# Kernel optimization log

Hardware: AMD Instinct MI355X
Metric: run time of the kernel (lower is better)

Reference implementation:

```python
import jax, jax.numpy as jnp
import numpy as np

D = 1024
H = 16
HD = D // H


def setup_inputs() -> dict:
    key = jax.random.key(0)
    ks = jax.random.split(key, 11)
    B, S = 4, 1024
    s = 0.02
    return {
        "q": jax.random.normal(ks[0], (B, S, D), jnp.float32),
        "k": jax.random.normal(ks[1], (B, S, D), jnp.float32),
        "v": jax.random.normal(ks[2], (B, S, D), jnp.float32),
        "Wq": jax.random.normal(ks[3], (D, D), jnp.float32) * s,
        "bq": jnp.zeros((D,), jnp.float32),
        "Wk": jax.random.normal(ks[4], (D, D), jnp.float32) * s,
        "bk": jnp.zeros((D,), jnp.float32),
        "Wv": jax.random.normal(ks[5], (D, D), jnp.float32) * s,
        "bv": jnp.zeros((D,), jnp.float32),
        "Wo": jax.random.normal(ks[6], (D, D), jnp.float32) * s,
        "bo": jnp.zeros((D,), jnp.float32),
    }


def _split_heads(x):
    # [B, S, D] -> [B, H, S, HD]
    B, S, _ = x.shape
    return x.reshape(B, S, H, HD).transpose(0, 2, 1, 3)


def reference(q, k, v, Wq, bq, Wk, bk, Wv, bv, Wo, bo):
    # Projections followed by ReLU (faithful to the original module)
    qh = _split_heads(jax.nn.relu(q @ Wq + bq))
    kh = _split_heads(jax.nn.relu(k @ Wk + bk))
    vh = _split_heads(jax.nn.relu(v @ Wv + bv))
    # NOTE: original scales by sqrt(input_dim), not sqrt(head_dim)
    scale = 1.0 / jnp.sqrt(jnp.float32(D))
    scores = jnp.einsum("bhsd,bhtd->bhst", qh, kh) * scale  # [B,H,S,S]
    weights = jax.nn.softmax(scores, axis=-1)  # dropout is identity in eval
    attn = jnp.einsum("bhst,bhtd->bhsd", weights, vh)  # [B,H,S,HD]
    B, _, S, _ = attn.shape
    attn = attn.transpose(0, 2, 1, 3).reshape(B, S, D)
    return attn @ Wo + bo
```

## Files before the change

kernel.cpp:

```cpp
#include <hip/hip_runtime.h>
#include <math.h>

#define Dm 1024
#define Hn 16
#define HDn 64
#define Sn 1024

typedef __attribute__((ext_vector_type(8))) __bf16 bf16x8;
typedef __attribute__((ext_vector_type(4))) float floatx4;

__device__ __forceinline__ void async_ld16(void* lds, const void* g) {
    __builtin_amdgcn_global_load_lds(
        (const __attribute__((address_space(1))) void*)g,
        (__attribute__((address_space(3))) void*)lds,
        16, 0, 0);
}

struct PrepArgs {
    const float* qkv[3];
    __bf16*      qkv_o[3];
    const float* W[4];
    __bf16*      WT[4];
    float*       out_zero;
};

__global__ __launch_bounds__(256) void prep_kernel(PrepArgs a)
{
    __shared__ float sT[64][65];
    const int z = blockIdx.z, x = blockIdx.x, tid = threadIdx.x;

    if (z < 3) {
        const float* src = a.qkv[z];
        __bf16* dst = a.qkv_o[z];
        const int lin = x * 256 + tid;
        const float4 v0 = ((const float4*)src)[lin * 2];
        const float4 v1 = ((const float4*)src)[lin * 2 + 1];
        bf16x8 o;
        o[0] = (__bf16)v0.x; o[1] = (__bf16)v0.y; o[2] = (__bf16)v0.z; o[3] = (__bf16)v0.w;
        o[4] = (__bf16)v1.x; o[5] = (__bf16)v1.y; o[6] = (__bf16)v1.z; o[7] = (__bf16)v1.w;
        ((bf16x8*)dst)[lin] = o;
    } else if (z < 7) {
        if (x >= 256) return;
        const float* W = a.W[z - 3];
        __bf16* O = a.WT[z - 3];
        const int bi = (x >> 4) * 64, bj = (x & 15) * 64;
        const int colr = tid & 63, rowg = tid >> 6;
        #pragma unroll
        for (int i = 0; i < 16; ++i) {
            const int kk = i * 4 + rowg;
            sT[kk][colr] = W[(size_t)(bi + kk) * Dm + bj + colr];
        }
        __syncthreads();
        #pragma unroll
        for (int i = 0; i < 16; ++i) {
            const int rn = i * 4 + rowg;
            O[(size_t)(bj + rn) * Dm + bi + colr] = (__bf16)sT[colr][rn];
        }
    } else {
        float4* o = (float4*)a.out_zero;
        const int i = (x * 256 + tid) * 2;
        const float4 zz = make_float4(0.f, 0.f, 0.f, 0.f);
        o[i] = zz;
        o[i + 1] = zz;
    }
}

struct GemmArgs {
    const __bf16* X[3];
    const __bf16* WT[3];
    const float*  bias[3];
    void*         out[3];
    int   layout[3];
    float esc[3];
};

__global__ __launch_bounds__(256) void gemm_bf16_kernel(GemmArgs args)
{
    __shared__ __align__(16) __bf16 sA[128 * 64];
    __shared__ __align__(16) __bf16 sB[128 * 64];

    const int z = blockIdx.z;
    const __bf16* __restrict__ Xb  = args.X[z];
    const __bf16* __restrict__ WTb = args.WT[z];
    const float*  __restrict__ bias = args.bias[z];
    void* __restrict__ outp = args.out[z];
    const int layout = args.layout[z];
    const float escale = args.esc[z];

    const int tid = threadIdx.x;
    const int id = blockIdx.x + (blockIdx.y << 3);
    const int bm = (((id & 7) << 2) | (id >> 6)) * 128;
    const int bn = ((id >> 3) & 7) * 128;

    const int lane = tid & 63;
    const int wave = tid >> 6;
    const int wm = (wave & 1) * 64;
    const int wn = (wave >> 1) * 64;
    const int l15 = lane & 15, quad = lane >> 4;

    floatx4 acc[4][4];
    #pragma unroll
    for (int mi = 0; mi < 4; ++mi)
        #pragma unroll
        for (int ni = 0; ni < 4; ++ni)
            acc[mi][ni] = (floatx4){0.f, 0.f, 0.f, 0.f};

    const __bf16* gA[4];
    const __bf16* gB[4];
    #pragma unroll
    for (int j = 0; j < 4; ++j) {
        const int c = j * 256 + tid;
        const int row = c >> 3;
        const int q = (c & 7) ^ (row & 7);
        gA[j] = Xb  + (size_t)(bm + row) * Dm + q * 8;
        gB[j] = WTb + (size_t)(bn + row) * Dm + q * 8;
    }
    char* const lA = (char*)sA + (tid & 192) * 16;
    char* const lB = (char*)sB + (tid & 192) * 16;

    for (int kt = 0; kt < Dm; kt += 64) {
        #pragma unroll
        for (int j = 0; j < 4; ++j) {
            async_ld16(lA + j * 4096, gA[j] + kt);
            async_ld16(lB + j * 4096, gB[j] + kt);
        }
        __syncthreads();

        #pragma unroll
        for (int ks = 0; ks < 2; ++ks) {
            bf16x8 af[4], bfr[4];
            #pragma unroll
            for (int mi = 0; mi < 4; ++mi) {
                const int r = wm + mi * 16 + l15;
                af[mi] = *(const bf16x8*)(sA + r * 64 + ((((ks << 2) + quad) ^ (r & 7)) * 8));
            }
            #pragma unroll
            for (int ni = 0; ni < 4; ++ni) {
                const int r = wn + ni * 16 + l15;
                bfr[ni] = *(const bf16x8*)(sB + r * 64 + ((((ks << 2) + quad) ^ (r & 7)) * 8));
            }
            #pragma unroll
            for (int mi = 0; mi < 4; ++mi)
                #pragma unroll
                for (int ni = 0; ni < 4; ++ni)
                    acc[mi][ni] = __builtin_amdgcn_mfma_f32_16x16x32_bf16(
                        af[mi], bfr[ni], acc[mi][ni], 0, 0, 0);
        }
        __syncthreads();
    }

    #pragma unroll
    for (int mi = 0; mi < 4; ++mi) {
        #pragma unroll
        for (int ni = 0; ni < 4; ++ni) {
            const int n = bn + wn + ni * 16 + l15;
            const float bv = bias[n];
            const int h = n >> 6, d = n & 63;
            #pragma unroll
            for (int reg = 0; reg < 4; ++reg) {
                const int m = bm + wm + mi * 16 + quad * 4 + reg;
                const int b = m >> 10, s = m & 1023;
                float v = fmaxf(acc[mi][ni][reg] + bv, 0.0f) * escale;
                if (layout == 0)
                    ((__bf16*)outp)[((size_t)(b * Hn + h) * 1024 + s) * 64 + d] = (__bf16)v;
                else
                    ((__bf16*)outp)[((size_t)(b * Hn + h) * 64 + d) * 1024 + s] = (__bf16)v;
            }
        }
    }
}

__global__ __launch_bounds__(256) void gemm_splitk_kernel(
    const __bf16* __restrict__ Xb, const __bf16* __restrict__ WTb,
    const float* __restrict__ bias, float* __restrict__ outp)
{
    __shared__ __align__(16) __bf16 sA[128 * 64];
    __shared__ __align__(16) __bf16 sB[128 * 64];

    const int tid = threadIdx.x;
    const int kz = blockIdx.z;
    const int id = blockIdx.x + (blockIdx.y << 3);
    const int bm = (((id & 7) << 2) | (id >> 6)) * 128;
    const int bn = ((id >> 3) & 7) * 128;

    const int lane = tid & 63;
    const int wave = tid >> 6;
    const int wm = (wave & 1) * 64;
    const int wn = (wave >> 1) * 64;
    const int l15 = lane & 15, quad = lane >> 4;

    floatx4 acc[4][4];
    #pragma unroll
    for (int mi = 0; mi < 4; ++mi)
        #pragma unroll
        for (int ni = 0; ni < 4; ++ni)
            acc[mi][ni] = (floatx4){0.f, 0.f, 0.f, 0.f};

    const int kofs = kz * 512;
    const __bf16* gA[4];
    const __bf16* gB[4];
    #pragma unroll
    for (int j = 0; j < 4; ++j) {
        const int c = j * 256 + tid;
        const int row = c >> 3;
        const int q = (c & 7) ^ (row & 7);
        gA[j] = Xb  + (size_t)(bm + row) * Dm + kofs + q * 8;
        gB[j] = WTb + (size_t)(bn + row) * Dm + kofs + q * 8;
    }
    char* const lA = (char*)sA + (tid & 192) * 16;
    char* const lB = (char*)sB + (tid & 192) * 16;

    for (int kt = 0; kt < 512; kt += 64) {
        #pragma unroll
        for (int j = 0; j < 4; ++j) {
            async_ld16(lA + j * 4096, gA[j] + kt);
            async_ld16(lB + j * 4096, gB[j] + kt);
        }
        __syncthreads();

        #pragma unroll
        for (int ks = 0; ks < 2; ++ks) {
            bf16x8 af[4], bfr[4];
            #pragma unroll
            for (int mi = 0; mi < 4; ++mi) {
                const int r = wm + mi * 16 + l15;
                af[mi] = *(const bf16x8*)(sA + r * 64 + ((((ks << 2) + quad) ^ (r & 7)) * 8));
            }
            #pragma unroll
            for (int ni = 0; ni < 4; ++ni) {
                const int r = wn + ni * 16 + l15;
                bfr[ni] = *(const bf16x8*)(sB + r * 64 + ((((ks << 2) + quad) ^ (r & 7)) * 8));
            }
            #pragma unroll
            for (int mi = 0; mi < 4; ++mi)
                #pragma unroll
                for (int ni = 0; ni < 4; ++ni)
                    acc[mi][ni] = __builtin_amdgcn_mfma_f32_16x16x32_bf16(
                        af[mi], bfr[ni], acc[mi][ni], 0, 0, 0);
        }
        __syncthreads();
    }

    #pragma unroll
    for (int mi = 0; mi < 4; ++mi) {
        #pragma unroll
        for (int ni = 0; ni < 4; ++ni) {
            const int n = bn + wn + ni * 16 + l15;
            const float bv = (kz == 0) ? bias[n] : 0.0f;
            #pragma unroll
            for (int reg = 0; reg < 4; ++reg) {
                const int m = bm + wm + mi * 16 + quad * 4 + reg;
                atomicAdd(outp + (size_t)m * 1024 + n, acc[mi][ni][reg] + bv);
            }
        }
    }
}

__global__ __launch_bounds__(256, 2) void flash_attn_kernel(
    const __bf16* __restrict__ Qh,
    const __bf16* __restrict__ Kh,
    const __bf16* __restrict__ Vt,
    __bf16* __restrict__ ctx)
{
    __shared__ __align__(16) char sKV[2][16384];
    __shared__ __align__(16) __bf16 sP[4][32 * 64];

    const int tid = threadIdx.x;
    const int wave = tid >> 6, lane = tid & 63;
    const int l15 = lane & 15, quad = lane >> 4;

    const int id = blockIdx.x + (blockIdx.y << 3) + (blockIdx.z << 7);
    const int kk = id >> 3;
    const int bh = ((id & 7) << 3) | (kk & 7);
    const int b = bh >> 4, h = bh & 15;
    const int qb = (kk >> 3) * 128 + wave * 32;

    bf16x8 aQ[2][2];
    #pragma unroll
    for (int mi = 0; mi < 2; ++mi)
        #pragma unroll
        for (int ks = 0; ks < 2; ++ks)
            aQ[mi][ks] = *(const bf16x8*)(Qh +
                (size_t)(bh * Sn + qb + mi * 16 + l15) * 64 + ks * 32 + quad * 8);

    const int s0 = tid, s1 = tid + 256;
    const int r0 = s0 >> 3, q0c = (s0 & 7) ^ (r0 & 7);
    const int r1 = s1 >> 3, q1c = (s1 & 7) ^ (r1 & 7);
    const __bf16* gK0 = Kh + (size_t)(bh * Sn + r0) * 64 + q0c * 8;
    const __bf16* gK1 = Kh + (size_t)(bh * Sn + r1) * 64 + q1c * 8;
    const __bf16* gV0 = Vt + (size_t)(bh * 64 + r0) * Sn + q0c * 8;
    const __bf16* gV1 = Vt + (size_t)(bh * 64 + r1) * Sn + q1c * 8;
    const int wofs = (tid & 192) * 16;

    floatx4 oacc[2][4];
    #pragma unroll
    for (int mi = 0; mi < 2; ++mi)
        #pragma unroll
        for (int nf = 0; nf < 4; ++nf)
            oacc[mi][nf] = (floatx4){0.f, 0.f, 0.f, 0.f};
    float lsum[2][4];
    #pragma unroll
    for (int mi = 0; mi < 2; ++mi)
        #pragma unroll
        for (int r = 0; r < 4; ++r) lsum[mi][r] = 0.0f;

    __bf16* sPw = sP[wave];

    {
        char* bK = sKV[0];
        char* bV = sKV[0] + 8192;
        async_ld16(bK + wofs,        gK0);
        async_ld16(bK + 4096 + wofs, gK1);
        async_ld16(bV + wofs,        gV0);
        async_ld16(bV + 4096 + wofs, gV1);
    }

    int cur = 0;
    for (int it = 0; it < 16; ++it) {
        __syncthreads();

        if (it + 1 < 16) {
            const int t0n = (it + 1) * 64;
            char* bK = sKV[cur ^ 1];
            char* bV = sKV[cur ^ 1] + 8192;
            async_ld16(bK + wofs,        gK0 + (size_t)t0n * 64);
            async_ld16(bK + 4096 + wofs, gK1 + (size_t)t0n * 64);
            async_ld16(bV + wofs,        gV0 + t0n);
            async_ld16(bV + 4096 + wofs, gV1 + t0n);
        }

        const __bf16* sK = (const __bf16*)sKV[cur];
        const __bf16* sV = (const __bf16*)(sKV[cur] + 8192);

        floatx4 sc[2][4];
        #pragma unroll
        for (int mi = 0; mi < 2; ++mi)
            #pragma unroll
            for (int nf = 0; nf < 4; ++nf)
                sc[mi][nf] = (floatx4){0.f, 0.f, 0.f, 0.f};
        #pragma unroll
        for (int ks = 0; ks < 2; ++ks) {
            bf16x8 bK[4];
            #pragma unroll
            for (int nf = 0; nf < 4; ++nf) {
                const int n = nf * 16 + l15;
                bK[nf] = *(const bf16x8*)(sK + (n * 8 + (((ks << 2) + quad) ^ (n & 7))) * 8);
            }
            #pragma unroll
            for (int mi = 0; mi < 2; ++mi)
                #pragma unroll
                for (int nf = 0; nf < 4; ++nf)
                    sc[mi][nf] = __builtin_amdgcn_mfma_f32_16x16x32_bf16(
                        aQ[mi][ks], bK[nf], sc[mi][nf], 0, 0, 0);
        }

        #pragma unroll
        for (int mi = 0; mi < 2; ++mi)
            #pragma unroll
            for (int nf = 0; nf < 4; ++nf) {
                const int t = nf * 16 + l15;
                #pragma unroll
                for (int r = 0; r < 4; ++r) {
                    const float p = __builtin_amdgcn_exp2f(fminf(sc[mi][nf][r], 126.0f));
                    const __bf16 pb = (__bf16)p;
                    lsum[mi][r] += (float)pb;
                    const int rr = mi * 16 + quad * 4 + r;
                    sPw[(rr * 8 + ((t >> 3) ^ (rr & 7))) * 8 + (t & 7)] = pb;
                }
            }

        #pragma unroll
        for (int ks = 0; ks < 2; ++ks) {
            bf16x8 aP[2], bV[4];
            #pragma unroll
            for (int mi = 0; mi < 2; ++mi) {
                const int r = mi * 16 + l15;
                aP[mi] = *(const bf16x8*)(sPw + (r * 8 + (((ks << 2) + quad) ^ (r & 7))) * 8);
            }
            #pragma unroll
            for (int nf = 0; nf < 4; ++nf) {
                const int n = nf * 16 + l15;
                bV[nf] = *(const bf16x8*)(sV + (n * 8 + (((ks << 2) + quad) ^ (n & 7))) * 8);
            }
            #pragma unroll
            for (int mi = 0; mi < 2; ++mi)
                #pragma unroll
                for (int nf = 0; nf < 4; ++nf)
                    oacc[mi][nf] = __builtin_amdgcn_mfma_f32_16x16x32_bf16(
                        aP[mi], bV[nf], oacc[mi][nf], 0, 0, 0);
        }

        cur ^= 1;
    }

    float linv[2][4];
    #pragma unroll
    for (int mi = 0; mi < 2; ++mi)
        #pragma unroll
        for (int r = 0; r < 4; ++r) {
            float l = lsum[mi][r];
            l += __shfl_xor(l, 1, 64);
            l += __shfl_xor(l, 2, 64);
            l += __shfl_xor(l, 4, 64);
            l += __shfl_xor(l, 8, 64);
            linv[mi][r] = 1.0f / l;
        }

    #pragma unroll
    for (int mi = 0; mi < 2; ++mi)
        #pragma unroll
        for (int nf = 0; nf < 4; ++nf) {
            const int d = h * 64 + nf * 16 + l15;
            #pragma unroll
            for (int reg = 0; reg < 4; ++reg) {
                const int s = qb + mi * 16 + quad * 4 + reg;
                ctx[(size_t)(b * Sn + s) * Dm + d] =
                    (__bf16)(oacc[mi][nf][reg] * linv[mi][reg]);
            }
        }
}

extern "C" void kernel_launch(void* const* d_in, const int* in_sizes, int n_in,
                              void* d_out, int out_size, void* d_ws, size_t ws_size,
                              hipStream_t stream)
{
    const float* q  = (const float*)d_in[0];
    const float* k  = (const float*)d_in[1];
    const float* v  = (const float*)d_in[2];
    const float* Wq = (const float*)d_in[3];
    const float* bq = (const float*)d_in[4];
    const float* Wk = (const float*)d_in[5];
    const float* bk = (const float*)d_in[6];
    const float* Wv = (const float*)d_in[7];
    const float* bv = (const float*)d_in[8];
    const float* Wo = (const float*)d_in[9];
    const float* bo = (const float*)d_in[10];

    char* ws = (char*)d_ws;
    const size_t MB = 1024 * 1024;
    __bf16* qb_ = (__bf16*)(ws);
    __bf16* kb_ = (__bf16*)(ws + 8 * MB);
    __bf16* vb_ = (__bf16*)(ws + 16 * MB);
    __bf16* WTq = (__bf16*)(ws + 24 * MB);
    __bf16* WTk = (__bf16*)(ws + 26 * MB);
    __bf16* WTv = (__bf16*)(ws + 28 * MB);
    __bf16* WTo = (__bf16*)(ws + 30 * MB);
    __bf16* Qh  = (__bf16*)(ws + 32 * MB);
    __bf16* Kh  = (__bf16*)(ws + 40 * MB);
    __bf16* Vt  = (__bf16*)(ws + 48 * MB);
    __bf16* ctx = (__bf16*)(ws + 56 * MB);

    PrepArgs pa;
    pa.qkv[0] = q; pa.qkv[1] = k; pa.qkv[2] = v;
    pa.qkv_o[0] = qb_; pa.qkv_o[1] = kb_; pa.qkv_o[2] = vb_;
    pa.W[0] = Wq; pa.W[1] = Wk; pa.W[2] = Wv; pa.W[3] = Wo;
    pa.WT[0] = WTq; pa.WT[1] = WTk; pa.WT[2] = WTv; pa.WT[3] = WTo;
    pa.out_zero = (float*)d_out;
    prep_kernel<<<dim3(2048, 1, 8), 256, 0, stream>>>(pa);

    const float QSCALE = 0.0450842200f;

    GemmArgs qkv;
    qkv.X[0] = qb_;  qkv.X[1] = kb_;  qkv.X[2] = vb_;
    qkv.WT[0] = WTq; qkv.WT[1] = WTk; qkv.WT[2] = WTv;
    qkv.bias[0] = bq; qkv.bias[1] = bk; qkv.bias[2] = bv;
    qkv.out[0] = Qh;  qkv.out[1] = Kh;  qkv.out[2] = Vt;
    qkv.layout[0] = 0; qkv.layout[1] = 0; qkv.layout[2] = 1;
    qkv.esc[0] = QSCALE; qkv.esc[1] = 1.0f; qkv.esc[2] = 1.0f;
    gemm_bf16_kernel<<<dim3(8, 32, 3), 256, 0, stream>>>(qkv);

    flash_attn_kernel<<<dim3(8, 16, 4), 256, 0, stream>>>(Qh, Kh, Vt, ctx);

    gemm_splitk_kernel<<<dim3(8, 32, 2), 256, 0, stream>>>(
        ctx, WTo, bo, (float*)d_out);
}
```

Measured before the change: 231.8 us.

## Fuse fp32-to-bf16 activation conversion into QKV GEMM LDS loads

```diff
diff --git a/kernel.cpp b/kernel.cpp
--- a/kernel.cpp
+++ b/kernel.cpp
@@ -17,8 +17,6 @@
 }
 
 struct PrepArgs {
-    const float* qkv[3];
-    __bf16*      qkv_o[3];
     const float* W[4];
     __bf16*      WT[4];
     float*       out_zero;
@@ -29,20 +27,10 @@
     __shared__ float sT[64][65];
     const int z = blockIdx.z, x = blockIdx.x, tid = threadIdx.x;
 
-    if (z < 3) {
-        const float* src = a.qkv[z];
-        __bf16* dst = a.qkv_o[z];
-        const int lin = x * 256 + tid;
-        const float4 v0 = ((const float4*)src)[lin * 2];
-        const float4 v1 = ((const float4*)src)[lin * 2 + 1];
-        bf16x8 o;
-        o[0] = (__bf16)v0.x; o[1] = (__bf16)v0.y; o[2] = (__bf16)v0.z; o[3] = (__bf16)v0.w;
-        o[4] = (__bf16)v1.x; o[5] = (__bf16)v1.y; o[6] = (__bf16)v1.z; o[7] = (__bf16)v1.w;
-        ((bf16x8*)dst)[lin] = o;
-    } else if (z < 7) {
+    if (z < 4) {
         if (x >= 256) return;
-        const float* W = a.W[z - 3];
-        __bf16* O = a.WT[z - 3];
+        const float* W = a.W[z];
+        __bf16* O = a.WT[z];
         const int bi = (x >> 4) * 64, bj = (x & 15) * 64;
         const int colr = tid & 63, rowg = tid >> 6;
         #pragma unroll
@@ -66,7 +54,7 @@
 }
 
 struct GemmArgs {
-    const __bf16* X[3];
+    const float*  X[3];
     const __bf16* WT[3];
     const float*  bias[3];
     void*         out[3];
@@ -76,11 +64,11 @@
 
 __global__ __launch_bounds__(256) void gemm_bf16_kernel(GemmArgs args)
 {
-    __shared__ __align__(16) __bf16 sA[128 * 64];
-    __shared__ __align__(16) __bf16 sB[128 * 64];
+    __shared__ __align__(16) float  sA[128 * 32];
+    __shared__ __align__(16) __bf16 sB[128 * 32];
 
     const int z = blockIdx.z;
-    const __bf16* __restrict__ Xb  = args.X[z];
+    const float*  __restrict__ Xb  = args.X[z];
     const __bf16* __restrict__ WTb = args.WT[z];
     const float*  __restrict__ bias = args.bias[z];
     void* __restrict__ outp = args.out[z];
@@ -105,47 +93,52 @@
         for (int ni = 0; ni < 4; ++ni)
             acc[mi][ni] = (floatx4){0.f, 0.f, 0.f, 0.f};
 
-    const __bf16* gA[4];
-    const __bf16* gB[4];
+    const float* gA[4];
     #pragma unroll
     for (int j = 0; j < 4; ++j) {
         const int c = j * 256 + tid;
-        const int row = c >> 3;
-        const int q = (c & 7) ^ (row & 7);
-        gA[j] = Xb  + (size_t)(bm + row) * Dm + q * 8;
-        gB[j] = WTb + (size_t)(bn + row) * Dm + q * 8;
-    }
+        const int row = c >> 3, cc = c & 7;
+        gA[j] = Xb + (size_t)(bm + row) * Dm + ((cc ^ (row & 7)) * 4);
+    }
+    const int c0 = tid,       r0 = c0 >> 2, q0 = (c0 & 3) ^ (r0 & 3);
+    const int c1 = tid + 256, r1 = c1 >> 2, q1 = (c1 & 3) ^ (r1 & 3);
+    const __bf16* gB0 = WTb + (size_t)(bn + r0) * Dm + q0 * 8;
+    const __bf16* gB1 = WTb + (size_t)(bn + r1) * Dm + q1 * 8;
     char* const lA = (char*)sA + (tid & 192) * 16;
     char* const lB = (char*)sB + (tid & 192) * 16;
 
-    for (int kt = 0; kt < Dm; kt += 64) {
-        #pragma unroll
-        for (int j = 0; j < 4; ++j) {
+    for (int kt = 0; kt < Dm; kt += 32) {
+        #pragma unroll
+        for (int j = 0; j < 4; ++j)
             async_ld16(lA + j * 4096, gA[j] + kt);
-            async_ld16(lB + j * 4096, gB[j] + kt);
-        }
-        __syncthreads();
-
-        #pragma unroll
-        for (int ks = 0; ks < 2; ++ks) {
-            bf16x8 af[4], bfr[4];
-            #pragma unroll
-            for (int mi = 0; mi < 4; ++mi) {
-                const int r = wm + mi * 16 + l15;
-                af[mi] = *(const bf16x8*)(sA + r * 64 + ((((ks << 2) + quad) ^ (r & 7)) * 8));
-            }
-            #pragma unroll
-            for (int ni = 0; ni < 4; ++ni) {
-                const int r = wn + ni * 16 + l15;
-                bfr[ni] = *(const bf16x8*)(sB + r * 64 + ((((ks << 2) + quad) ^ (r & 7)) * 8));
-            }
-            #pragma unroll
-            for (int mi = 0; mi < 4; ++mi)
-                #pragma unroll
-                for (int ni = 0; ni < 4; ++ni)
-                    acc[mi][ni] = __builtin_amdgcn_mfma_f32_16x16x32_bf16(
-                        af[mi], bfr[ni], acc[mi][ni], 0, 0, 0);
-        }
+        async_ld16(lB,        gB0 + kt);
+        async_ld16(lB + 4096, gB1 + kt);
+        __syncthreads();
+
+        bf16x8 af[4], bfr[4];
+        #pragma unroll
+        for (int mi = 0; mi < 4; ++mi) {
+            const int r = wm + mi * 16 + l15;
+            const int s0_ = (2 * quad) ^ (r & 7);
+            const int s1_ = (2 * quad + 1) ^ (r & 7);
+            const floatx4 fa0 = *(const floatx4*)(sA + r * 32 + s0_ * 4);
+            const floatx4 fa1 = *(const floatx4*)(sA + r * 32 + s1_ * 4);
+            af[mi][0] = (__bf16)fa0[0]; af[mi][1] = (__bf16)fa0[1];
+            af[mi][2] = (__bf16)fa0[2]; af[mi][3] = (__bf16)fa0[3];
+            af[mi][4] = (__bf16)fa1[0]; af[mi][5] = (__bf16)fa1[1];
+            af[mi][6] = (__bf16)fa1[2]; af[mi][7] = (__bf16)fa1[3];
+        }
+        #pragma unroll
+        for (int ni = 0; ni < 4; ++ni) {
+            const int r = wn + ni * 16 + l15;
+            bfr[ni] = *(const bf16x8*)(sB + r * 32 + ((quad ^ (r & 3)) * 8));
+        }
+        #pragma unroll
+        for (int mi = 0; mi < 4; ++mi)
+            #pragma unroll
+            for (int ni = 0; ni < 4; ++ni)
+                acc[mi][ni] = __builtin_amdgcn_mfma_f32_16x16x32_bf16(
+                    af[mi], bfr[ni], acc[mi][ni], 0, 0, 0);
         __syncthreads();
     }
 
@@ -438,9 +431,6 @@
 
     char* ws = (char*)d_ws;
     const size_t MB = 1024 * 1024;
-    __bf16* qb_ = (__bf16*)(ws);
-    __bf16* kb_ = (__bf16*)(ws + 8 * MB);
-    __bf16* vb_ = (__bf16*)(ws + 16 * MB);
     __bf16* WTq = (__bf16*)(ws + 24 * MB);
     __bf16* WTk = (__bf16*)(ws + 26 * MB);
     __bf16* WTv = (__bf16*)(ws + 28 * MB);
@@ -451,17 +441,15 @@
     __bf16* ctx = (__bf16*)(ws + 56 * MB);
 
     PrepArgs pa;
-    pa.qkv[0] = q; pa.qkv[1] = k; pa.qkv[2] = v;
-    pa.qkv_o[0] = qb_; pa.qkv_o[1] = kb_; pa.qkv_o[2] = vb_;
     pa.W[0] = Wq; pa.W[1] = Wk; pa.W[2] = Wv; pa.W[3] = Wo;
     pa.WT[0] = WTq; pa.WT[1] = WTk; pa.WT[2] = WTv; pa.WT[3] = WTo;
     pa.out_zero = (float*)d_out;
-    prep_kernel<<<dim3(2048, 1, 8), 256, 0, stream>>>(pa);
+    prep_kernel<<<dim3(2048, 1, 5), 256, 0, stream>>>(pa);
 
     const float QSCALE = 0.0450842200f;
 
     GemmArgs qkv;
-    qkv.X[0] = qb_;  qkv.X[1] = kb_;  qkv.X[2] = vb_;
+    qkv.X[0] = q;   qkv.X[1] = k;   qkv.X[2] = v;
     qkv.WT[0] = WTq; qkv.WT[1] = WTk; qkv.WT[2] = WTv;
     qkv.bias[0] = bq; qkv.bias[1] = bk; qkv.bias[2] = bv;
     qkv.out[0] = Qh;  qkv.out[1] = Kh;  qkv.out[2] = Vt;
```

New measurement: 244.9 us. 1.06x slower.

## Rewrite QKV projection GEMM as 256x256-tile 8-phase pipelined kernel

Applied to the files above, without the earlier changes.

```diff
diff --git a/kernel.cpp b/kernel.cpp
--- a/kernel.cpp
+++ b/kernel.cpp
@@ -74,91 +74,146 @@
     float esc[3];
 };
 
-__global__ __launch_bounds__(256) void gemm_bf16_kernel(GemmArgs args)
+__global__ __launch_bounds__(512, 2) void gemm_qkv_8ph(GemmArgs args)
 {
-    __shared__ __align__(16) __bf16 sA[128 * 64];
-    __shared__ __align__(16) __bf16 sB[128 * 64];
-
-    const int z = blockIdx.z;
-    const __bf16* __restrict__ Xb  = args.X[z];
-    const __bf16* __restrict__ WTb = args.WT[z];
+    __shared__ __align__(16) char ldsA[65536];
+    __shared__ __align__(16) char ldsB[65536];
+
+    const int bid = blockIdx.x;
+    const int wg  = (bid & 7) * 24 + (bid >> 3);
+    const int z   = wg >> 6;
+    const int rr_ = wg & 63;
+    const int bm  = (rr_ & 15) << 8;
+    const int bn  = (rr_ >> 4) << 8;
+
+    const __bf16* __restrict__ Xb   = args.X[z];
+    const __bf16* __restrict__ WTb  = args.WT[z];
     const float*  __restrict__ bias = args.bias[z];
     void* __restrict__ outp = args.out[z];
     const int layout = args.layout[z];
     const float escale = args.esc[z];
 
-    const int tid = threadIdx.x;
-    const int id = blockIdx.x + (blockIdx.y << 3);
-    const int bm = (((id & 7) << 2) | (id >> 6)) * 128;
-    const int bn = ((id >> 3) & 7) * 128;
-
-    const int lane = tid & 63;
-    const int wave = tid >> 6;
-    const int wm = (wave & 1) * 64;
-    const int wn = (wave >> 1) * 64;
-    const int l15 = lane & 15, quad = lane >> 4;
-
-    floatx4 acc[4][4];
-    #pragma unroll
-    for (int mi = 0; mi < 4; ++mi)
+    const int tid  = threadIdx.x;
+    const int lane = tid & 63, wave = tid >> 6;
+    const int wm8  = wave >> 2;
+    const int wn8  = wave & 3;
+    const int l15  = lane & 15, quad = lane >> 4;
+
+    floatx4 acc[8][4];
+    #pragma unroll
+    for (int mi = 0; mi < 8; ++mi)
         #pragma unroll
         for (int ni = 0; ni < 4; ++ni)
             acc[mi][ni] = (floatx4){0.f, 0.f, 0.f, 0.f};
 
-    const __bf16* gA[4];
-    const __bf16* gB[4];
-    #pragma unroll
-    for (int j = 0; j < 4; ++j) {
-        const int c = j * 256 + tid;
-        const int row = c >> 3;
-        const int q = (c & 7) ^ (row & 7);
-        gA[j] = Xb  + (size_t)(bm + row) * Dm + q * 8;
-        gB[j] = WTb + (size_t)(bn + row) * Dm + q * 8;
-    }
-    char* const lA = (char*)sA + (tid & 192) * 16;
-    char* const lB = (char*)sB + (tid & 192) * 16;
-
-    for (int kt = 0; kt < Dm; kt += 64) {
-        #pragma unroll
-        for (int j = 0; j < 4; ++j) {
-            async_ld16(lA + j * 4096, gA[j] + kt);
-            async_ld16(lB + j * 4096, gB[j] + kt);
-        }
-        __syncthreads();
-
-        #pragma unroll
-        for (int ks = 0; ks < 2; ++ks) {
-            bf16x8 af[4], bfr[4];
-            #pragma unroll
-            for (int mi = 0; mi < 4; ++mi) {
-                const int r = wm + mi * 16 + l15;
-                af[mi] = *(const bf16x8*)(sA + r * 64 + ((((ks << 2) + quad) ^ (r & 7)) * 8));
-            }
-            #pragma unroll
-            for (int ni = 0; ni < 4; ++ni) {
-                const int r = wn + ni * 16 + l15;
-                bfr[ni] = *(const bf16x8*)(sB + r * 64 + ((((ks << 2) + quad) ^ (r & 7)) * 8));
-            }
-            #pragma unroll
-            for (int mi = 0; mi < 4; ++mi)
+    const int p0 = tid >> 3;
+    const int g0 = (tid & 7) ^ (p0 & 7);
+    const __bf16* gA = Xb  + (size_t)(bm + p0) * Dm + g0 * 8;
+    const __bf16* gB = WTb + (size_t)(bn + p0) * Dm + g0 * 8;
+    const int ldsw = wave * 1024;
+
+    auto STAGE = [&](char* arena, int buf, int half, const __bf16* gbase, int tk) {
+        char* d = arena + (((buf << 1) + half) << 14) + ldsw;
+        const __bf16* s = gbase + (size_t)half * 128 * Dm + tk * 64;
+        async_ld16(d,        s);
+        async_ld16(d + 8192, s + 64 * Dm);
+    };
+    auto LDA = [&](bf16x8* aq, int buf, int miBase) {
+        const char* base = ldsA + (((buf << 1) + wm8) << 14);
+        #pragma unroll
+        for (int m = 0; m < 2; ++m) {
+            const int p = (miBase + m) * 16 + l15;
+            #pragma unroll
+            for (int ks = 0; ks < 2; ++ks)
+                aq[m * 2 + ks] = *(const bf16x8*)(base + p * 128 +
+                    ((((ks << 2) | quad)) ^ (p & 7)) * 16);
+        }
+    };
+    auto LDB = [&](bf16x8 (*bb)[2], int buf) {
+        const char* base = ldsB + (((buf << 1) + (wn8 >> 1)) << 14);
+        #pragma unroll
+        for (int n = 0; n < 4; ++n) {
+            const int p = (wn8 & 1) * 64 + n * 16 + l15;
+            #pragma unroll
+            for (int ks = 0; ks < 2; ++ks)
+                bb[n][ks] = *(const bf16x8*)(base + p * 128 +
+                    ((((ks << 2) | quad)) ^ (p & 7)) * 16);
+        }
+    };
+    auto MF = [&](const bf16x8* aq, bf16x8 (*bb)[2], int miBase) {
+        __builtin_amdgcn_s_setprio(1);
+        #pragma unroll
+        for (int m = 0; m < 2; ++m)
+            #pragma unroll
+            for (int n = 0; n < 4; ++n)
                 #pragma unroll
-                for (int ni = 0; ni < 4; ++ni)
-                    acc[mi][ni] = __builtin_amdgcn_mfma_f32_16x16x32_bf16(
-                        af[mi], bfr[ni], acc[mi][ni], 0, 0, 0);
-        }
-        __syncthreads();
-    }
-
-    #pragma unroll
-    for (int mi = 0; mi < 4; ++mi) {
-        #pragma unroll
-        for (int ni = 0; ni < 4; ++ni) {
-            const int n = bn + wn + ni * 16 + l15;
-            const float bv = bias[n];
-            const int h = n >> 6, d = n & 63;
+                for (int ks = 0; ks < 2; ++ks)
+                    acc[miBase + m][n] = __builtin_amdgcn_mfma_f32_16x16x32_bf16(
+                        aq[m * 2 + ks], bb[n][ks], acc[miBase + m][n], 0, 0, 0);
+        __builtin_amdgcn_s_setprio(0);
+    };
+
+#define PH_MID() do { __builtin_amdgcn_s_barrier(); \
+    asm volatile("s_waitcnt lgkmcnt(0)" ::: "memory"); \
+    __builtin_amdgcn_sched_barrier(0); } while (0)
+#define PH_END() do { __builtin_amdgcn_s_barrier(); \
+    __builtin_amdgcn_sched_barrier(0); } while (0)
+#define VMW4()   do { asm volatile("s_waitcnt vmcnt(4)" ::: "memory"); } while (0)
+
+    STAGE(ldsA, 0, 0, gA, 0);  STAGE(ldsA, 0, 1, gA, 0);
+    STAGE(ldsB, 0, 0, gB, 0);  STAGE(ldsB, 0, 1, gB, 0);
+    STAGE(ldsB, 1, 0, gB, 1);  STAGE(ldsB, 1, 1, gB, 1);
+    VMW4();
+    __builtin_amdgcn_s_barrier();
+    __builtin_amdgcn_sched_barrier(0);
+
+    bf16x8 bb[4][2];
+    bf16x8 aq[4];
+
+    for (int it = 0; it < 8; ++it) {
+        const int T = it << 1;
+        LDB(bb, 0); LDA(aq, 0, 0);
+        STAGE(ldsA, 1, 0, gA, T + 1);
+        PH_MID(); MF(aq, bb, 0); PH_END();
+        LDA(aq, 0, 2);
+        STAGE(ldsA, 1, 1, gA, T + 1);
+        PH_MID(); MF(aq, bb, 2); PH_END();
+        LDA(aq, 0, 4);
+        STAGE(ldsB, 0, 0, gB, (T + 2) & 15);
+        PH_MID(); MF(aq, bb, 4); PH_END();
+        LDA(aq, 0, 6);
+        STAGE(ldsB, 0, 1, gB, (T + 2) & 15);
+        VMW4();
+        PH_MID(); MF(aq, bb, 6); PH_END();
+        LDB(bb, 1); LDA(aq, 1, 0);
+        STAGE(ldsA, 0, 0, gA, (T + 2) & 15);
+        PH_MID(); MF(aq, bb, 0); PH_END();
+        LDA(aq, 1, 2);
+        STAGE(ldsA, 0, 1, gA, (T + 2) & 15);
+        PH_MID(); MF(aq, bb, 2); PH_END();
+        LDA(aq, 1, 4);
+        STAGE(ldsB, 1, 0, gB, (T + 3) & 15);
+        PH_MID(); MF(aq, bb, 4); PH_END();
+        LDA(aq, 1, 6);
+        STAGE(ldsB, 1, 1, gB, (T + 3) & 15);
+        VMW4();
+        PH_MID(); MF(aq, bb, 6); PH_END();
+    }
+
+#undef PH_MID
+#undef PH_END
+#undef VMW4
+
+    #pragma unroll
+    for (int ni = 0; ni < 4; ++ni) {
+        const int n = bn + wn8 * 64 + ni * 16 + l15;
+        const float bv = bias[n];
+        const int h = n >> 6, d = n & 63;
+        #pragma unroll
+        for (int mi = 0; mi < 8; ++mi) {
             #pragma unroll
             for (int reg = 0; reg < 4; ++reg) {
-                const int m = bm + wm + mi * 16 + quad * 4 + reg;
+                const int m = bm + wm8 * 128 + mi * 16 + quad * 4 + reg;
                 const int b = m >> 10, s = m & 1023;
                 float v = fmaxf(acc[mi][ni][reg] + bv, 0.0f) * escale;
                 if (layout == 0)
@@ -467,7 +522,7 @@
     qkv.out[0] = Qh;  qkv.out[1] = Kh;  qkv.out[2] = Vt;
     qkv.layout[0] = 0; qkv.layout[1] = 0; qkv.layout[2] = 1;
     qkv.esc[0] = QSCALE; qkv.esc[1] = 1.0f; qkv.esc[2] = 1.0f;
-    gemm_bf16_kernel<<<dim3(8, 32, 3), 256, 0, stream>>>(qkv);
+    gemm_qkv_8ph<<<dim3(192, 1, 1), 512, 0, stream>>>(qkv);
 
     flash_attn_kernel<<<dim3(8, 16, 4), 256, 0, stream>>>(Qh, Kh, Vt, ctx);
 
```

Measured after the change: 249.9 us. 7.8% more time.
